# Kernel optimization log

Measured on AMD Instinct MI355X. Metric: run time of the kernel, lower is better.

## Reference

```python
import jax, jax.numpy as jnp
import numpy as np


def setup_inputs() -> dict:
    key = jax.random.key(0)
    k1, k2, k3 = jax.random.split(key, 3)
    vol_shape = (4, 1, 128, 192, 192)   # [B, C, D, H, W]
    dsc_shape = (4, 1, 8, 12, 12)       # PatchGAN-style discriminator logits
    return {
        "dsc_fake": jax.random.normal(k1, dsc_shape, dtype=jnp.float32),
        "predicts": jax.random.normal(k2, vol_shape, dtype=jnp.float32),
        "y_data": jax.random.normal(k3, vol_shape, dtype=jnp.float32),
        "zeros": jnp.zeros(dsc_shape, dtype=jnp.float32),
    }


def reference(dsc_fake, predicts, y_data, zeros):
    # BCE with logits (stable form), target = zeros
    bce = jnp.mean(
        jnp.maximum(dsc_fake, 0.0) - dsc_fake * zeros
        + jnp.log1p(jnp.exp(-jnp.abs(dsc_fake)))
    )
    # L1 loss between target volume and prediction
    g_loss_l1 = jnp.mean(jnp.abs(y_data - predicts))
    # Finite-difference gradient MSE along D, H, W (axes 2,3,4).
    # Original detaches to numpy, so this term carries no gradient.
    yd = jax.lax.stop_gradient(y_data)
    pr = jax.lax.stop_gradient(predicts)
    g_loss_gd = jnp.float32(0.0)
    for ax in (2, 3, 4):
        gy = jnp.abs(jnp.gradient(yd, axis=ax))   # central diff interior, one-sided edges
        gp = jnp.abs(jnp.gradient(pr, axis=ax))
        g_loss_gd = g_loss_gd + jnp.mean((gy - gp) ** 2)
    return bce + 100.0 * g_loss_l1 + 100.0 * g_loss_gd
```

## Files before the change

kernel.cpp:

```cpp
#include <hip/hip_runtime.h>
#include <math.h>

namespace {
constexpr int BATCH = 4;
constexpr int DDIM  = 128;
constexpr int HDIM  = 192;
constexpr int WDIM  = 192;
constexpr long long NTOT = (long long)BATCH * DDIM * HDIM * WDIM;
constexpr int NDSC  = 4 * 1 * 8 * 12 * 12;

constexpr int HT     = 12;
constexpr int DT     = 16;
constexpr int ROWS   = HT + 2;
constexpr int SLABF  = ROWS * WDIM;
constexpr int SLAB2  = 2 * SLABF;
constexpr int BLOCKV = 192;
constexpr int GRIDV  = BATCH * (DDIM / DT) * (HDIM / HT);
constexpr int UPW    = 7;
constexpr int PLSTR  = HDIM * WDIM;
constexpr int BLOCKF = 256;
}

#define GTERM(dy, dp, s2) { float t0_ = fabsf(dy) - fabsf(dp); gd = fmaf(t0_ * t0_, (s2), gd); }

#define STAGE(buf, plane)                                                      \
    {                                                                          \
        const int poff_ = (plane) * PLSTR;                                     \
        _Pragma("unroll")                                                      \
        for (int k = 0; k < UPW; ++k) {                                        \
            __builtin_amdgcn_global_load_lds(                                  \
                (const __attribute__((address_space(1))) void*)(sr[k] + poff_),\
                (__attribute__((address_space(3))) void*)(                     \
                    &slab[buf][0] + (wv * UPW + k) * 256),                     \
                16, 0, 0);                                                     \
        }                                                                      \
    }

__global__ __launch_bounds__(BLOCKV) void vol_kernel(const float* __restrict__ p,
                                                     const float* __restrict__ y,
                                                     float* __restrict__ part) {
    __shared__ float slab[3][SLAB2];
    __shared__ float red[2][3];

    const int tid  = threadIdx.x;
    const int wv   = tid >> 6;
    const int lane = tid & 63;
    const int r    = tid >> 4;
    const int i16  = tid & 15;
    const int w0   = i16 * 12;

    const int blk = blockIdx.x;
    const int ht = blk & 15;
    const int dc = (blk >> 4) & 7;
    const int b  = blk >> 7;
    const int h0 = ht * HT;
    const int d0 = dc * DT;
    const int h  = h0 + r;

    const float* sr[UPW];
    #pragma unroll
    for (int k = 0; k < UPW; ++k) {
        const int u   = wv * UPW + k;
        const int fi  = u * 256 + lane * 4;
        const int ts  = fi >= SLABF;
        const int fj  = ts ? fi - SLABF : fi;
        const int row = fj / WDIM;
        const int col = fj - row * WDIM;
        int hrow = h0 - 1 + row;
        hrow = hrow < 0 ? 0 : (hrow > HDIM - 1 ? HDIM - 1 : hrow);
        sr[k] = (ts ? p : y) + (b * DDIM * HDIM + hrow) * WDIM + col;
    }

    float4 ym[2][3], yc[2][3];
    {
        const int pmz = d0 ? d0 - 1 : 0;
        const int om = ((b * DDIM + pmz) * HDIM + h) * WDIM + w0;
        const int oc = ((b * DDIM + d0 ) * HDIM + h) * WDIM + w0;
        #pragma unroll
        for (int g = 0; g < 3; ++g) {
            ym[0][g] = *(const float4*)(y + om + 4 * g);
            ym[1][g] = *(const float4*)(p + om + 4 * g);
            yc[0][g] = *(const float4*)(y + oc + 4 * g);
            yc[1][g] = *(const float4*)(p + oc + 4 * g);
        }
    }
    STAGE(0, d0);
    STAGE(1, d0 + 1);
    STAGE(2, d0 + 2);

    float l1 = 0.f, gd = 0.f;
    const float s2h  = (h == 0 || h == HDIM - 1) ? 1.f : 0.25f;
    const float s2w0 = (i16 == 0)  ? 1.f : 0.25f;
    const float s2w3 = (i16 == 15) ? 1.f : 0.25f;

    int cur = 0;
    #pragma unroll 1
    for (int i = 0; i < DT; ++i) {
        const int e = d0 + i;
        if (i == DT - 1) { asm volatile("s_waitcnt vmcnt(0)" ::: "memory"); }
        else             { asm volatile("s_waitcnt vmcnt(7)" ::: "memory"); }
        __builtin_amdgcn_sched_barrier(0);
        __builtin_amdgcn_s_barrier();
        __builtin_amdgcn_sched_barrier(0);

        const int nxt = (cur == 2) ? 0 : cur + 1;
        const float* cs = &slab[cur][0];
        const float* ns = &slab[nxt][0];
        const float s2d = (e == 0 || e == DDIM - 1) ? 1.f : 0.25f;

        const int rowc = (r + 1) * WDIM;
        const float wlY = cs[rowc + (i16 ? w0 - 1 : 0)];
        const float wrY = cs[rowc + (i16 < 15 ? w0 + 12 : WDIM - 1)];
        const float wlP = cs[SLABF + rowc + (i16 ? w0 - 1 : 0)];
        const float wrP = cs[SLABF + rowc + (i16 < 15 ? w0 + 12 : WDIM - 1)];

        float4 cn[2][3];
        #pragma unroll
        for (int g = 0; g < 3; ++g) {
            const int off = w0 + 4 * g;
            const float4 cny = *(const float4*)&ns[rowc + off];
            const float4 cnp = *(const float4*)&ns[SLABF + rowc + off];
            const float4 hmy = *(const float4*)&cs[r * WDIM + off];
            const float4 hpy = *(const float4*)&cs[(r + 2) * WDIM + off];
            const float4 hmp = *(const float4*)&cs[SLABF + r * WDIM + off];
            const float4 hpp = *(const float4*)&cs[SLABF + (r + 2) * WDIM + off];
            cn[0][g] = cny; cn[1][g] = cnp;
            const float4 ay = yc[0][g], ap = yc[1][g];
            const float4 my = ym[0][g], mp = ym[1][g];

            l1 += fabsf(ay.x - ap.x) + fabsf(ay.y - ap.y)
                + fabsf(ay.z - ap.z) + fabsf(ay.w - ap.w);
            GTERM(hpy.x - hmy.x, hpp.x - hmp.x, s2h);
            GTERM(hpy.y - hmy.y, hpp.y - hmp.y, s2h);
            GTERM(hpy.z - hmy.z, hpp.z - hmp.z, s2h);
            GTERM(hpy.w - hmy.w, hpp.w - hmp.w, s2h);
            GTERM(cny.x - my.x, cnp.x - mp.x, s2d);
            GTERM(cny.y - my.y, cnp.y - mp.y, s2d);
            GTERM(cny.z - my.z, cnp.z - mp.z, s2d);
            GTERM(cny.w - my.w, cnp.w - mp.w, s2d);
        }
        {
            const float4 a0 = yc[0][0], a1 = yc[0][1], a2 = yc[0][2];
            const float4 p0 = yc[1][0], p1 = yc[1][1], p2 = yc[1][2];
            GTERM(a0.y - wlY , p0.y - wlP , s2w0);
            GTERM(a0.z - a0.x, p0.z - p0.x, 0.25f);
            GTERM(a0.w - a0.y, p0.w - p0.y, 0.25f);
            GTERM(a1.x - a0.z, p1.x - p0.z, 0.25f);
            GTERM(a1.y - a0.w, p1.y - p0.w, 0.25f);
            GTERM(a1.z - a1.x, p1.z - p1.x, 0.25f);
            GTERM(a1.w - a1.y, p1.w - p1.y, 0.25f);
            GTERM(a2.x - a1.z, p2.x - p1.z, 0.25f);
            GTERM(a2.y - a1.w, p2.y - p1.w, 0.25f);
            GTERM(a2.z - a2.x, p2.z - p2.x, 0.25f);
            GTERM(a2.w - a2.y, p2.w - p2.y, 0.25f);
            GTERM(wrY  - a2.z, wrP  - p2.z, s2w3);
        }
        #pragma unroll
        for (int g = 0; g < 3; ++g) {
            ym[0][g] = yc[0][g]; ym[1][g] = yc[1][g];
            yc[0][g] = cn[0][g]; yc[1][g] = cn[1][g];
        }

        __builtin_amdgcn_sched_barrier(0);
        asm volatile("s_waitcnt lgkmcnt(0)" ::: "memory");
        __builtin_amdgcn_sched_barrier(0);
        __builtin_amdgcn_s_barrier();
        __builtin_amdgcn_sched_barrier(0);
        if (i <= DT - 3) {
            int pl = d0 + i + 3; if (pl > DDIM - 1) pl = DDIM - 1;
            STAGE(cur, pl);
        }
        cur = nxt;
    }

    #pragma unroll
    for (int off = 32; off > 0; off >>= 1) {
        l1 += __shfl_down(l1, off, 64);
        gd += __shfl_down(gd, off, 64);
    }
    if (lane == 0) { red[0][wv] = l1; red[1][wv] = gd; }
    __syncthreads();
    if (tid == 0) {
        part[2 * blk]     = red[0][0] + red[0][1] + red[0][2];
        part[2 * blk + 1] = red[1][0] + red[1][1] + red[1][2];
    }
}

__global__ __launch_bounds__(BLOCKF) void finalize_kernel(const float* __restrict__ dsc,
                                                          const float* __restrict__ part,
                                                          float* __restrict__ out) {
    float l1 = 0.f, gd = 0.f, s = 0.f;
    for (int i = threadIdx.x; i < GRIDV; i += BLOCKF) {
        l1 += part[2 * i];
        gd += part[2 * i + 1];
    }
    for (int i = threadIdx.x; i < NDSC; i += BLOCKF) {
        const float x = dsc[i];
        s += fmaxf(x, 0.f) + log1pf(expf(-fabsf(x)));
    }
    __shared__ float a[4], c[4], e2[4];
    #pragma unroll
    for (int off = 32; off > 0; off >>= 1) {
        l1 += __shfl_down(l1, off, 64);
        gd += __shfl_down(gd, off, 64);
        s  += __shfl_down(s,  off, 64);
    }
    if ((threadIdx.x & 63) == 0) {
        const int w = threadIdx.x >> 6;
        a[w] = l1; c[w] = gd; e2[w] = s;
    }
    __syncthreads();
    if (threadIdx.x == 0) {
        const float bce = (e2[0] + e2[1] + e2[2] + e2[3]) / (float)NDSC;
        const float l1m = (a[0] + a[1] + a[2] + a[3]) / (float)NTOT;
        const float gdm = (c[0] + c[1] + c[2] + c[3]) / (float)NTOT;
        out[0] = bce + 100.f * (l1m + gdm);
    }
}

extern "C" void kernel_launch(void* const* d_in, const int* in_sizes, int n_in,
                              void* d_out, int out_size, void* d_ws, size_t ws_size,
                              hipStream_t stream) {
    const float* dsc_fake = (const float*)d_in[0];
    const float* predicts = (const float*)d_in[1];
    const float* y_data   = (const float*)d_in[2];
    float* part = (float*)d_ws;
    float* out  = (float*)d_out;

    vol_kernel<<<GRIDV, BLOCKV, 0, stream>>>(predicts, y_data, part);
    finalize_kernel<<<1, BLOCKF, 0, stream>>>(dsc_fake, part, out);
}
```

Measured before the change: 190.2 us.

## Use single-wave blocks with a 5-deep LDS ring to drop block barriers

Changes each block to one 64-lane wave covering a 4-row by 32-plane tile. LDS staging becomes a 5-slot ring prefetching 4 planes ahead, which lets the per-iteration s_barrier and lgkmcnt waits go away because only one wave touches LDS. Block indices are swizzled across 8 groups, and the cross-wave shared-memory reduction is replaced by a direct per-wave write. The trade-off is more halo rows reloaded per output row (6 loaded for 4 computed instead of 14 for 12), a larger grid, and a longer D-loop per block.

Measured after the change: 196.0 us. 1.03x slower.

```diff
diff --git a/kernel.cpp b/kernel.cpp
--- a/kernel.cpp
+++ b/kernel.cpp
@@ -9,59 +9,59 @@
 constexpr long long NTOT = (long long)BATCH * DDIM * HDIM * WDIM;
 constexpr int NDSC  = 4 * 1 * 8 * 12 * 12;
 
-constexpr int HT     = 12;
-constexpr int DT     = 16;
+constexpr int HT     = 4;
+constexpr int DT     = 32;
 constexpr int ROWS   = HT + 2;
 constexpr int SLABF  = ROWS * WDIM;
 constexpr int SLAB2  = 2 * SLABF;
-constexpr int BLOCKV = 192;
-constexpr int GRIDV  = BATCH * (DDIM / DT) * (HDIM / HT);
-constexpr int UPW    = 7;
+constexpr int RING   = 5;
+constexpr int UNITS  = (SLAB2 * 4) / 1024;
+constexpr int BLOCKV = 64;
+constexpr int NHT    = HDIM / HT;
+constexpr int NDC    = DDIM / DT;
+constexpr int GRIDV  = BATCH * NDC * NHT;
 constexpr int PLSTR  = HDIM * WDIM;
 constexpr int BLOCKF = 256;
 }
 
 #define GTERM(dy, dp, s2) { float t0_ = fabsf(dy) - fabsf(dp); gd = fmaf(t0_ * t0_, (s2), gd); }
 
-#define STAGE(buf, plane)                                                      \
-    {                                                                          \
-        const int poff_ = (plane) * PLSTR;                                     \
-        _Pragma("unroll")                                                      \
-        for (int k = 0; k < UPW; ++k) {                                        \
-            __builtin_amdgcn_global_load_lds(                                  \
-                (const __attribute__((address_space(1))) void*)(sr[k] + poff_),\
-                (__attribute__((address_space(3))) void*)(                     \
-                    &slab[buf][0] + (wv * UPW + k) * 256),                     \
-                16, 0, 0);                                                     \
-        }                                                                      \
+#define STAGE(buf, plane)                                                       \
+    {                                                                           \
+        const int poff_ = (plane) * PLSTR;                                      \
+        _Pragma("unroll")                                                       \
+        for (int k = 0; k < UNITS; ++k) {                                       \
+            __builtin_amdgcn_global_load_lds(                                   \
+                (const __attribute__((address_space(1))) void*)(sr[k] + poff_), \
+                (__attribute__((address_space(3))) void*)(&slab[buf][k * 256]), \
+                16, 0, 0);                                                      \
+        }                                                                       \
     }
 
 __global__ __launch_bounds__(BLOCKV) void vol_kernel(const float* __restrict__ p,
                                                      const float* __restrict__ y,
                                                      float* __restrict__ part) {
-    __shared__ float slab[3][SLAB2];
-    __shared__ float red[2][3];
-
-    const int tid  = threadIdx.x;
-    const int wv   = tid >> 6;
-    const int lane = tid & 63;
-    const int r    = tid >> 4;
-    const int i16  = tid & 15;
+    __shared__ float slab[RING][SLAB2];
+
+    const int lane = threadIdx.x;
+    const int r    = lane >> 4;
+    const int i16  = lane & 15;
     const int w0   = i16 * 12;
 
-    const int blk = blockIdx.x;
-    const int ht = blk & 15;
-    const int dc = (blk >> 4) & 7;
-    const int b  = blk >> 7;
-    const int h0 = ht * HT;
-    const int d0 = dc * DT;
-    const int h  = h0 + r;
-
-    const float* sr[UPW];
+    const int blk0 = blockIdx.x;
+    const int swz  = (blk0 & 7) * (GRIDV / 8) + (blk0 >> 3);
+    const int ht   = swz % NHT;
+    const int rs   = swz / NHT;
+    const int dc   = rs & (NDC - 1);
+    const int b    = rs >> 2;
+    const int h0   = ht * HT;
+    const int d0   = dc * DT;
+    const int h    = h0 + r;
+
+    const float* sr[UNITS];
     #pragma unroll
-    for (int k = 0; k < UPW; ++k) {
-        const int u   = wv * UPW + k;
-        const int fi  = u * 256 + lane * 4;
+    for (int k = 0; k < UNITS; ++k) {
+        const int fi  = k * 256 + lane * 4;
         const int ts  = fi >= SLABF;
         const int fj  = ts ? fi - SLABF : fi;
         const int row = fj / WDIM;
@@ -87,6 +87,7 @@
     STAGE(0, d0);
     STAGE(1, d0 + 1);
     STAGE(2, d0 + 2);
+    STAGE(3, d0 + 3);
 
     float l1 = 0.f, gd = 0.f;
     const float s2h  = (h == 0 || h == HDIM - 1) ? 1.f : 0.25f;
@@ -97,15 +98,20 @@
     #pragma unroll 1
     for (int i = 0; i < DT; ++i) {
         const int e = d0 + i;
-        if (i == DT - 1) { asm volatile("s_waitcnt vmcnt(0)" ::: "memory"); }
-        else             { asm volatile("s_waitcnt vmcnt(7)" ::: "memory"); }
+        if (i < DT - 2)       { asm volatile("s_waitcnt vmcnt(18)" ::: "memory"); }
+        else if (i == DT - 2) { asm volatile("s_waitcnt vmcnt(9)"  ::: "memory"); }
+        else                  { asm volatile("s_waitcnt vmcnt(0)"  ::: "memory"); }
         __builtin_amdgcn_sched_barrier(0);
-        __builtin_amdgcn_s_barrier();
-        __builtin_amdgcn_sched_barrier(0);
-
-        const int nxt = (cur == 2) ? 0 : cur + 1;
+
+        if (i <= DT - 4) {
+            int pl = e + 4; if (pl > DDIM - 1) pl = DDIM - 1;
+            const int stg = cur ? cur - 1 : RING - 1;
+            STAGE(stg, pl);
+        }
+
+        const int nx = (cur + 1 == RING) ? 0 : cur + 1;
         const float* cs = &slab[cur][0];
-        const float* ns = &slab[nxt][0];
+        const float* ns = &slab[nx][0];
         const float s2d = (e == 0 || e == DDIM - 1) ? 1.f : 0.25f;
 
         const int rowc = (r + 1) * WDIM;
@@ -160,17 +166,7 @@
             ym[0][g] = yc[0][g]; ym[1][g] = yc[1][g];
             yc[0][g] = cn[0][g]; yc[1][g] = cn[1][g];
         }
-
-        __builtin_amdgcn_sched_barrier(0);
-        asm volatile("s_waitcnt lgkmcnt(0)" ::: "memory");
-        __builtin_amdgcn_sched_barrier(0);
-        __builtin_amdgcn_s_barrier();
-        __builtin_amdgcn_sched_barrier(0);
-        if (i <= DT - 3) {
-            int pl = d0 + i + 3; if (pl > DDIM - 1) pl = DDIM - 1;
-            STAGE(cur, pl);
-        }
-        cur = nxt;
+        cur = nx;
     }
 
     #pragma unroll
@@ -178,11 +174,9 @@
         l1 += __shfl_down(l1, off, 64);
         gd += __shfl_down(gd, off, 64);
     }
-    if (lane == 0) { red[0][wv] = l1; red[1][wv] = gd; }
-    __syncthreads();
-    if (tid == 0) {
-        part[2 * blk]     = red[0][0] + red[0][1] + red[0][2];
-        part[2 * blk + 1] = red[1][0] + red[1][1] + red[1][2];
+    if (lane == 0) {
+        part[2 * blk0]     = l1;
+        part[2 * blk0 + 1] = gd;
     }
 }
 
```
